# Kernel optimization log

Measured on AMD Instinct MI355X. Metric: run time of the kernel, lower is better.

The kernel has to match this reference:

```python
import jax, jax.numpy as jnp
import numpy as np

DIM = 4096
N_HEADS = 32
N_KV_HEADS = 8
HEAD_DIM = DIM // N_HEADS  # 128
N_REP = N_HEADS // N_KV_HEADS  # 4
MAX_BS = 16
MAX_SEQ = 4096
SEQLEN = 1
START_POS = 4095
ROPE_THETA = 500000.0


def setup_inputs() -> dict:
    key = jax.random.key(0)
    ks = jax.random.split(key, 8)
    w_scale = 0.02  # keep logits in a sane range
    x = jax.random.normal(ks[0], (MAX_BS, SEQLEN, DIM), dtype=jnp.float32)
    wq = jax.random.normal(ks[1], (DIM, N_HEADS * HEAD_DIM), dtype=jnp.float32) * w_scale
    wk = jax.random.normal(ks[2], (DIM, N_KV_HEADS * HEAD_DIM), dtype=jnp.float32) * w_scale
    wv = jax.random.normal(ks[3], (DIM, N_KV_HEADS * HEAD_DIM), dtype=jnp.float32) * w_scale
    wo = jax.random.normal(ks[4], (N_HEADS * HEAD_DIM, DIM), dtype=jnp.float32) * w_scale
    cache_k = jax.random.normal(ks[5], (MAX_BS, MAX_SEQ, N_KV_HEADS, HEAD_DIM), dtype=jnp.float32)
    cache_v = jax.random.normal(ks[6], (MAX_BS, MAX_SEQ, N_KV_HEADS, HEAD_DIM), dtype=jnp.float32)
    # true rotary frequencies for positions [START_POS, START_POS+SEQLEN)
    inv_freq = 1.0 / (ROPE_THETA ** (np.arange(0, HEAD_DIM, 2, dtype=np.float32) / HEAD_DIM))  # [hd/2]
    t = np.arange(START_POS, START_POS + SEQLEN, dtype=np.float32)[:, None]  # [s,1]
    angles = t * inv_freq[None, :]  # [s, hd/2]
    freqs_cos = jnp.asarray(np.cos(angles), dtype=jnp.float32)
    freqs_sin = jnp.asarray(np.sin(angles), dtype=jnp.float32)
    return {"x": x, "wq": wq, "wk": wk, "wv": wv, "wo": wo,
            "cache_k": cache_k, "cache_v": cache_v,
            "freqs_cos": freqs_cos, "freqs_sin": freqs_sin,
            "start_pos": START_POS}


def _rope(t, cos, sin):
    # t: [b, s, h, hd]; cos/sin: [s, hd/2] -> broadcast [1, s, 1, hd/2]
    b, s, h, hd = t.shape
    tp = t.reshape(b, s, h, hd // 2, 2)
    e, o = tp[..., 0], tp[..., 1]
    c = cos[None, :, None, :]
    sn = sin[None, :, None, :]
    re = e * c - o * sn
    im = e * sn + o * c
    return jnp.stack([re, im], axis=-1).reshape(b, s, h, hd)


def reference(x, wq, wk, wv, wo, cache_k, cache_v, freqs_cos, freqs_sin, start_pos):
    bsz, seqlen, _ = x.shape
    xq = (x @ wq).reshape(bsz, seqlen, N_HEADS, HEAD_DIM)
    xk = (x @ wk).reshape(bsz, seqlen, N_KV_HEADS, HEAD_DIM)
    xv = (x @ wv).reshape(bsz, seqlen, N_KV_HEADS, HEAD_DIM)
    xq = _rope(xq, freqs_cos, freqs_sin)
    xk = _rope(xk, freqs_cos, freqs_sin)
    # KV-cache append
    cache_k = jax.lax.dynamic_update_slice(cache_k, xk, (0, start_pos, 0, 0))
    cache_v = jax.lax.dynamic_update_slice(cache_v, xv, (0, start_pos, 0, 0))
    kv_len = start_pos + seqlen  # static Python int
    keys = cache_k[:, :kv_len]    # [b, t, g, hd]
    values = cache_v[:, :kv_len]  # [b, t, g, hd]
    # GQA via broadcasting (math-equivalent to repeat_kv)
    q = xq.reshape(bsz, seqlen, N_KV_HEADS, N_REP, HEAD_DIM)
    scale = 1.0 / jnp.sqrt(jnp.float32(HEAD_DIM))
    scores = jnp.einsum('bsgrh,btgh->bgrst', q, keys) * scale  # [b,g,r,s,t]
    probs = jax.nn.softmax(scores.astype(jnp.float32), axis=-1).astype(xq.dtype)
    out = jnp.einsum('bgrst,btgh->bsgrh', probs, values)  # [b,s,g,r,hd]
    out = out.reshape(bsz, seqlen, N_HEADS * HEAD_DIM)
    return out @ wo
```

## Files before the change

kernel.cpp:

```cpp
#include <hip/hip_runtime.h>
#include <math.h>

#define DIM    4096
#define NH     32
#define NKV    8
#define HD     128
#define BS     16
#define KVLEN  4096
#define LASTPOS 4095
#define QKV_COLS 6144
#define SS_STR 520

#define WS_QKV   0
#define WS_ATTN  98304
#define WS_PART  163840

__global__ __launch_bounds__(256) void zero_ws(
    float* __restrict__ qkv, float* __restrict__ out) {
  int i = blockIdx.x * 256 + threadIdx.x;
  float4 z = make_float4(0.f, 0.f, 0.f, 0.f);
  if (i < 24576) ((float4*)qkv)[i] = z;
  else           ((float4*)out)[i - 24576] = z;
}

__global__ __launch_bounds__(256) void qkv_proj(
    const float* __restrict__ x, const float* __restrict__ wq,
    const float* __restrict__ wk, const float* __restrict__ wv,
    float* __restrict__ qkv) {
  __shared__ float xs[16 * 64];
  const int tid = threadIdx.x;
  const int col = (blockIdx.x * 256 + tid) * 2;
  const int k0 = blockIdx.y * 64;

  for (int i = tid; i < 1024; i += 256) {
    int b = i >> 6, k = i & 63;
    xs[i] = x[b * DIM + k0 + k];
  }
  __syncthreads();

  const float* w;
  int wstride, wcol;
  if (col < 4096)      { w = wq; wstride = 4096; wcol = col; }
  else if (col < 5120) { w = wk; wstride = 1024; wcol = col - 4096; }
  else                 { w = wv; wstride = 1024; wcol = col - 5120; }
  const float* wp = w + (size_t)k0 * wstride + wcol;

  float acc0[16], acc1[16];
#pragma unroll
  for (int b = 0; b < 16; ++b) { acc0[b] = 0.f; acc1[b] = 0.f; }

#pragma unroll 2
  for (int k = 0; k < 64; k += 4) {
    float2 w0 = *(const float2*)(wp + (size_t)(k + 0) * wstride);
    float2 w1 = *(const float2*)(wp + (size_t)(k + 1) * wstride);
    float2 w2 = *(const float2*)(wp + (size_t)(k + 2) * wstride);
    float2 w3 = *(const float2*)(wp + (size_t)(k + 3) * wstride);
#pragma unroll
    for (int b = 0; b < 16; ++b) {
      float4 xb = *(const float4*)(&xs[b * 64 + k]);
      acc0[b] += xb.x * w0.x + xb.y * w1.x + xb.z * w2.x + xb.w * w3.x;
      acc1[b] += xb.x * w0.y + xb.y * w1.y + xb.z * w2.y + xb.w * w3.y;
    }
  }
#pragma unroll
  for (int b = 0; b < 16; ++b) {
    atomicAdd(&qkv[b * QKV_COLS + col],     acc0[b]);
    atomicAdd(&qkv[b * QKV_COLS + col + 1], acc1[b]);
  }
}

__global__ __launch_bounds__(256) void rope_kernel(
    float* __restrict__ qkv, const float* __restrict__ fc,
    const float* __restrict__ fs) {
  int t = blockIdx.x * 256 + threadIdx.x;
  if (t >= 16 * 40 * 64) return;
  int i  = t & 63;
  int hh = (t >> 6) % 40;
  int b  = t / (40 * 64);
  float c = fc[i], s = fs[i];
  int base;
  float scale;
  if (hh < 32) { base = b * QKV_COLS + hh * 128 + 2 * i; scale = 0.08838834764831845f; }
  else         { base = b * QKV_COLS + 4096 + (hh - 32) * 128 + 2 * i; scale = 1.0f; }
  float e = qkv[base], o = qkv[base + 1];
  qkv[base]     = (e * c - o * s) * scale;
  qkv[base + 1] = (e * s + o * c) * scale;
}

__global__ __launch_bounds__(512, 4) void attn_partial(
    const float* __restrict__ cache_k, const float* __restrict__ cache_v,
    const float* __restrict__ qkv, float* __restrict__ part) {
  __shared__ float qs[512];
  __shared__ float ss[4 * SS_STR];
  __shared__ float pacc[8][4][128];
  const int tid = threadIdx.x;
  const int w = tid >> 6, lane = tid & 63;
  const int p = lane >> 4, ql = lane & 15;
  const int chunk = blockIdx.x & 7;
  const int bg = blockIdx.x >> 3;
  const int b = bg >> 3, g = bg & 7;

  qs[tid] = qkv[b * QKV_COLS + g * 512 + tid];
  __syncthreads();

  float4 qA[4], qB[4];
#pragma unroll
  for (int h = 0; h < 4; ++h) {
    qA[h] = *(const float4*)(&qs[h * 128 + ql * 8]);
    qB[h] = *(const float4*)(&qs[h * 128 + ql * 8 + 4]);
  }

  const int t0 = chunk * 512;
  const float* kbase = cache_k + ((size_t)b * 4096 * 8 + g) * 128;
  const float* xk    = qkv + b * QKV_COLS + 4096 + g * 128;

  for (int it = 0; it < 16; ++it) {
    int r = w * 64 + it * 4 + p;
    int t = t0 + r;
    const float* krow = (t == LASTPOS) ? xk : (kbase + (size_t)t * 1024);
    float4 k0 = *(const float4*)(krow + ql * 8);
    float4 k1 = *(const float4*)(krow + ql * 8 + 4);
    float s[4];
#pragma unroll
    for (int h = 0; h < 4; ++h) {
      s[h] = k0.x * qA[h].x + k0.y * qA[h].y + k0.z * qA[h].z + k0.w * qA[h].w
           + k1.x * qB[h].x + k1.y * qB[h].y + k1.z * qB[h].z + k1.w * qB[h].w;
    }
#pragma unroll
    for (int off = 1; off < 16; off <<= 1) {
#pragma unroll
      for (int h = 0; h < 4; ++h) s[h] += __shfl_xor(s[h], off);
    }
    float v = (ql == 0) ? s[0] : (ql == 1) ? s[1] : (ql == 2) ? s[2] : s[3];
    if (ql < 4) ss[ql * SS_STR + r] = v;
  }
  __syncthreads();

  float* prow = part + ((size_t)(bg * 8 + chunk) * 4 + (w & 3)) * 130;
  if (w < 4) {
    float vals[8];
    float m = -1e30f;
#pragma unroll
    for (int i = 0; i < 8; ++i) {
      vals[i] = ss[w * SS_STR + lane + 64 * i];
      m = fmaxf(m, vals[i]);
    }
#pragma unroll
    for (int off = 1; off < 64; off <<= 1) m = fmaxf(m, __shfl_xor(m, off));
    float l = 0.f;
#pragma unroll
    for (int i = 0; i < 8; ++i) {
      float pe = __expf(vals[i] - m);
      ss[w * SS_STR + lane + 64 * i] = pe;
      l += pe;
    }
#pragma unroll
    for (int off = 1; off < 64; off <<= 1) l += __shfl_xor(l, off);
    if (lane == 0) { prow[128] = m; prow[129] = l; }
  }
  __syncthreads();

  const float* vbase = cache_v + ((size_t)b * 4096 * 8 + g) * 128;
  const float* xv    = qkv + b * QKV_COLS + 5120 + g * 128;
  const int h2 = lane >> 5;
  const int dq = lane & 31;
  float4 acc[4];
#pragma unroll
  for (int h = 0; h < 4; ++h) acc[h] = make_float4(0.f, 0.f, 0.f, 0.f);

#pragma unroll 2
  for (int j = 0; j < 32; ++j) {
    int r = w * 64 + 2 * j + h2;
    int t = t0 + r;
    const float* vrow = (t == LASTPOS) ? xv : (vbase + (size_t)t * 1024);
    float4 vv = *(const float4*)(vrow + dq * 4);
    float p0 = ss[0 * SS_STR + r];
    float p1 = ss[1 * SS_STR + r];
    float p2 = ss[2 * SS_STR + r];
    float p3 = ss[3 * SS_STR + r];
    acc[0].x += p0 * vv.x; acc[0].y += p0 * vv.y; acc[0].z += p0 * vv.z; acc[0].w += p0 * vv.w;
    acc[1].x += p1 * vv.x; acc[1].y += p1 * vv.y; acc[1].z += p1 * vv.z; acc[1].w += p1 * vv.w;
    acc[2].x += p2 * vv.x; acc[2].y += p2 * vv.y; acc[2].z += p2 * vv.z; acc[2].w += p2 * vv.w;
    acc[3].x += p3 * vv.x; acc[3].y += p3 * vv.y; acc[3].z += p3 * vv.z; acc[3].w += p3 * vv.w;
  }
#pragma unroll
  for (int h = 0; h < 4; ++h) {
    acc[h].x += __shfl_xor(acc[h].x, 32);
    acc[h].y += __shfl_xor(acc[h].y, 32);
    acc[h].z += __shfl_xor(acc[h].z, 32);
    acc[h].w += __shfl_xor(acc[h].w, 32);
  }
  if (lane < 32) {
#pragma unroll
    for (int h = 0; h < 4; ++h)
      *(float4*)(&pacc[w][h][dq * 4]) = acc[h];
  }
  __syncthreads();

  {
    int h = tid >> 7, d = tid & 127;
    float sum = 0.f;
#pragma unroll
    for (int w2 = 0; w2 < 8; ++w2) sum += pacc[w2][h][d];
    part[((size_t)(bg * 8 + chunk) * 4 + h) * 130 + d] = sum;
  }
}

__global__ __launch_bounds__(256) void attn_combine(
    const float* __restrict__ part, float* __restrict__ attn_out) {
  int t = blockIdx.x * 256 + threadIdx.x;
  int d = t & 127, r = (t >> 7) & 3, bg = t >> 9;
  int b = bg >> 3, g = bg & 7;
  float ms[8];
  float M = -1e30f;
#pragma unroll
  for (int c = 0; c < 8; ++c) {
    ms[c] = part[((size_t)(bg * 8 + c) * 4 + r) * 130 + 128];
    M = fmaxf(M, ms[c]);
  }
  float num = 0.f, den = 0.f;
#pragma unroll
  for (int c = 0; c < 8; ++c) {
    const float* prow = part + ((size_t)(bg * 8 + c) * 4 + r) * 130;
    float wgt = __expf(ms[c] - M);
    num += wgt * prow[d];
    den += wgt * prow[129];
  }
  attn_out[b * DIM + (g * 4 + r) * 128 + d] = num / den;
}

__global__ __launch_bounds__(256) void out_proj(
    const float* __restrict__ attn, const float* __restrict__ wo,
    float* __restrict__ out) {
  __shared__ float xs[16 * 64];
  const int tid = threadIdx.x;
  const int col = blockIdx.x * 256 + tid;
  const int k0 = blockIdx.y * 64;

  for (int i = tid; i < 1024; i += 256) {
    int b = i >> 6, k = i & 63;
    xs[i] = attn[b * DIM + k0 + k];
  }
  __syncthreads();

  const float* wp = wo + (size_t)k0 * 4096 + col;
  float acc[16];
#pragma unroll
  for (int b = 0; b < 16; ++b) acc[b] = 0.f;

#pragma unroll 2
  for (int k = 0; k < 64; k += 4) {
    float w0 = wp[(size_t)(k + 0) * 4096];
    float w1 = wp[(size_t)(k + 1) * 4096];
    float w2 = wp[(size_t)(k + 2) * 4096];
    float w3 = wp[(size_t)(k + 3) * 4096];
#pragma unroll
    for (int b = 0; b < 16; ++b) {
      float4 xb = *(const float4*)(&xs[b * 64 + k]);
      acc[b] += xb.x * w0 + xb.y * w1 + xb.z * w2 + xb.w * w3;
    }
  }
#pragma unroll
  for (int b = 0; b < 16; ++b) atomicAdd(&out[b * DIM + col], acc[b]);
}

extern "C" void kernel_launch(void* const* d_in, const int* in_sizes, int n_in,
                              void* d_out, int out_size, void* d_ws, size_t ws_size,
                              hipStream_t stream) {
  const float* x  = (const float*)d_in[0];
  const float* wq = (const float*)d_in[1];
  const float* wk = (const float*)d_in[2];
  const float* wv = (const float*)d_in[3];
  const float* wo = (const float*)d_in[4];
  const float* ck = (const float*)d_in[5];
  const float* cv = (const float*)d_in[6];
  const float* fc = (const float*)d_in[7];
  const float* fs = (const float*)d_in[8];

  float* ws_f  = (float*)d_ws;
  float* qkv   = ws_f + WS_QKV;
  float* attn  = ws_f + WS_ATTN;
  float* part  = ws_f + WS_PART;
  float* out   = (float*)d_out;

  zero_ws<<<160, 256, 0, stream>>>(qkv, out);
  qkv_proj<<<dim3(12, 64), 256, 0, stream>>>(x, wq, wk, wv, qkv);
  rope_kernel<<<160, 256, 0, stream>>>(qkv, fc, fs);
  attn_partial<<<1024, 512, 0, stream>>>(ck, cv, qkv, part);
  attn_combine<<<256, 256, 0, stream>>>(part, attn);
  out_proj<<<dim3(16, 64), 256, 0, stream>>>(attn, wo, out);
}
```

Measured before the change: 202.8 us.

## Replace atomic split-K with partial buffers and reduce kernels, halve attention chunk

```diff
diff --git a/kernel.cpp b/kernel.cpp
--- a/kernel.cpp
+++ b/kernel.cpp
@@ -9,28 +9,26 @@
 #define KVLEN  4096
 #define LASTPOS 4095
 #define QKV_COLS 6144
-#define SS_STR 520
+#define CHUNK  256
+#define NCH    16
+#define SS_STR 264
+#define NKC    64
 
 #define WS_QKV   0
 #define WS_ATTN  98304
 #define WS_PART  163840
-
-__global__ __launch_bounds__(256) void zero_ws(
-    float* __restrict__ qkv, float* __restrict__ out) {
-  int i = blockIdx.x * 256 + threadIdx.x;
-  float4 z = make_float4(0.f, 0.f, 0.f, 0.f);
-  if (i < 24576) ((float4*)qkv)[i] = z;
-  else           ((float4*)out)[i - 24576] = z;
-}
-
-__global__ __launch_bounds__(256) void qkv_proj(
+#define WS_PQ    1228800
+#define WS_PW    7520256
+
+__global__ __launch_bounds__(256) void qkv_projA(
     const float* __restrict__ x, const float* __restrict__ wq,
     const float* __restrict__ wk, const float* __restrict__ wv,
-    float* __restrict__ qkv) {
+    float* __restrict__ pq) {
   __shared__ float xs[16 * 64];
   const int tid = threadIdx.x;
   const int col = (blockIdx.x * 256 + tid) * 2;
-  const int k0 = blockIdx.y * 64;
+  const int kc = blockIdx.y;
+  const int k0 = kc * 64;
 
   for (int i = tid; i < 1024; i += 256) {
     int b = i >> 6, k = i & 63;
@@ -64,30 +62,34 @@
   }
 #pragma unroll
   for (int b = 0; b < 16; ++b) {
-    atomicAdd(&qkv[b * QKV_COLS + col],     acc0[b]);
-    atomicAdd(&qkv[b * QKV_COLS + col + 1], acc1[b]);
-  }
-}
-
-__global__ __launch_bounds__(256) void rope_kernel(
-    float* __restrict__ qkv, const float* __restrict__ fc,
-    const float* __restrict__ fs) {
+    *(float2*)(&pq[((size_t)kc * 16 + b) * QKV_COLS + col]) = make_float2(acc0[b], acc1[b]);
+  }
+}
+
+__global__ __launch_bounds__(256) void qkv_projB(
+    const float* __restrict__ pq, float* __restrict__ qkv,
+    const float* __restrict__ fc, const float* __restrict__ fs) {
   int t = blockIdx.x * 256 + threadIdx.x;
-  if (t >= 16 * 40 * 64) return;
-  int i  = t & 63;
-  int hh = (t >> 6) % 40;
-  int b  = t / (40 * 64);
-  float c = fc[i], s = fs[i];
-  int base;
-  float scale;
-  if (hh < 32) { base = b * QKV_COLS + hh * 128 + 2 * i; scale = 0.08838834764831845f; }
-  else         { base = b * QKV_COLS + 4096 + (hh - 32) * 128 + 2 * i; scale = 1.0f; }
-  float e = qkv[base], o = qkv[base + 1];
-  qkv[base]     = (e * c - o * s) * scale;
-  qkv[base + 1] = (e * s + o * c) * scale;
-}
-
-__global__ __launch_bounds__(512, 4) void attn_partial(
+  int b = t / 3072, pr = t % 3072;
+  int col = 2 * pr;
+  float e = 0.f, o = 0.f;
+#pragma unroll 8
+  for (int kc = 0; kc < NKC; ++kc) {
+    float2 v = *(const float2*)(&pq[((size_t)kc * 16 + b) * QKV_COLS + col]);
+    e += v.x; o += v.y;
+  }
+  float re = e, im = o;
+  if (col < 5120) {
+    int i = (col & 127) >> 1;
+    float c = fc[i], s = fs[i];
+    float scale = (col < 4096) ? 0.08838834764831845f : 1.0f;
+    re = (e * c - o * s) * scale;
+    im = (e * s + o * c) * scale;
+  }
+  *(float2*)(&qkv[b * QKV_COLS + col]) = make_float2(re, im);
+}
+
+__global__ __launch_bounds__(512, 8) void attn_partial(
     const float* __restrict__ cache_k, const float* __restrict__ cache_v,
     const float* __restrict__ qkv, float* __restrict__ part) {
   __shared__ float qs[512];
@@ -96,8 +98,8 @@
   const int tid = threadIdx.x;
   const int w = tid >> 6, lane = tid & 63;
   const int p = lane >> 4, ql = lane & 15;
-  const int chunk = blockIdx.x & 7;
-  const int bg = blockIdx.x >> 3;
+  const int chunk = blockIdx.x & 15;
+  const int bg = blockIdx.x >> 4;
   const int b = bg >> 3, g = bg & 7;
 
   qs[tid] = qkv[b * QKV_COLS + g * 512 + tid];
@@ -110,12 +112,13 @@
     qB[h] = *(const float4*)(&qs[h * 128 + ql * 8 + 4]);
   }
 
-  const int t0 = chunk * 512;
+  const int t0 = chunk * CHUNK;
   const float* kbase = cache_k + ((size_t)b * 4096 * 8 + g) * 128;
   const float* xk    = qkv + b * QKV_COLS + 4096 + g * 128;
 
-  for (int it = 0; it < 16; ++it) {
-    int r = w * 64 + it * 4 + p;
+#pragma unroll 1
+  for (int it = 0; it < 8; ++it) {
+    int r = w * 32 + it * 4 + p;
     int t = t0 + r;
     const float* krow = (t == LASTPOS) ? xk : (kbase + (size_t)t * 1024);
     float4 k0 = *(const float4*)(krow + ql * 8);
@@ -136,12 +139,12 @@
   }
   __syncthreads();
 
-  float* prow = part + ((size_t)(bg * 8 + chunk) * 4 + (w & 3)) * 130;
+  float* prow = part + ((size_t)(bg * NCH + chunk) * 4 + (w & 3)) * 130;
   if (w < 4) {
-    float vals[8];
+    float vals[4];
     float m = -1e30f;
 #pragma unroll
-    for (int i = 0; i < 8; ++i) {
+    for (int i = 0; i < 4; ++i) {
       vals[i] = ss[w * SS_STR + lane + 64 * i];
       m = fmaxf(m, vals[i]);
     }
@@ -149,7 +152,7 @@
     for (int off = 1; off < 64; off <<= 1) m = fmaxf(m, __shfl_xor(m, off));
     float l = 0.f;
 #pragma unroll
-    for (int i = 0; i < 8; ++i) {
+    for (int i = 0; i < 4; ++i) {
       float pe = __expf(vals[i] - m);
       ss[w * SS_STR + lane + 64 * i] = pe;
       l += pe;
@@ -168,9 +171,9 @@
 #pragma unroll
   for (int h = 0; h < 4; ++h) acc[h] = make_float4(0.f, 0.f, 0.f, 0.f);
 
-#pragma unroll 2
-  for (int j = 0; j < 32; ++j) {
-    int r = w * 64 + 2 * j + h2;
+#pragma unroll 4
+  for (int j = 0; j < 16; ++j) {
+    int r = w * 32 + 2 * j + h2;
     int t = t0 + r;
     const float* vrow = (t == LASTPOS) ? xv : (vbase + (size_t)t * 1024);
     float4 vv = *(const float4*)(vrow + dq * 4);
@@ -202,7 +205,7 @@
     float sum = 0.f;
 #pragma unroll
     for (int w2 = 0; w2 < 8; ++w2) sum += pacc[w2][h][d];
-    part[((size_t)(bg * 8 + chunk) * 4 + h) * 130 + d] = sum;
+    part[((size_t)(bg * NCH + chunk) * 4 + h) * 130 + d] = sum;
   }
 }
 
@@ -211,17 +214,17 @@
   int t = blockIdx.x * 256 + threadIdx.x;
   int d = t & 127, r = (t >> 7) & 3, bg = t >> 9;
   int b = bg >> 3, g = bg & 7;
-  float ms[8];
   float M = -1e30f;
-#pragma unroll
-  for (int c = 0; c < 8; ++c) {
-    ms[c] = part[((size_t)(bg * 8 + c) * 4 + r) * 130 + 128];
+  float ms[NCH];
+#pragma unroll
+  for (int c = 0; c < NCH; ++c) {
+    ms[c] = part[((size_t)(bg * NCH + c) * 4 + r) * 130 + 128];
     M = fmaxf(M, ms[c]);
   }
   float num = 0.f, den = 0.f;
 #pragma unroll
-  for (int c = 0; c < 8; ++c) {
-    const float* prow = part + ((size_t)(bg * 8 + c) * 4 + r) * 130;
+  for (int c = 0; c < NCH; ++c) {
+    const float* prow = part + ((size_t)(bg * NCH + c) * 4 + r) * 130;
     float wgt = __expf(ms[c] - M);
     num += wgt * prow[d];
     den += wgt * prow[129];
@@ -229,13 +232,14 @@
   attn_out[b * DIM + (g * 4 + r) * 128 + d] = num / den;
 }
 
-__global__ __launch_bounds__(256) void out_proj(
+__global__ __launch_bounds__(256) void out_projA(
     const float* __restrict__ attn, const float* __restrict__ wo,
-    float* __restrict__ out) {
+    float* __restrict__ pw) {
   __shared__ float xs[16 * 64];
   const int tid = threadIdx.x;
-  const int col = blockIdx.x * 256 + tid;
-  const int k0 = blockIdx.y * 64;
+  const int col = (blockIdx.x * 256 + tid) * 2;
+  const int kc = blockIdx.y;
+  const int k0 = kc * 64;
 
   for (int i = tid; i < 1024; i += 256) {
     int b = i >> 6, k = i & 63;
@@ -244,24 +248,38 @@
   __syncthreads();
 
   const float* wp = wo + (size_t)k0 * 4096 + col;
-  float acc[16];
-#pragma unroll
-  for (int b = 0; b < 16; ++b) acc[b] = 0.f;
+  float acc0[16], acc1[16];
+#pragma unroll
+  for (int b = 0; b < 16; ++b) { acc0[b] = 0.f; acc1[b] = 0.f; }
 
 #pragma unroll 2
   for (int k = 0; k < 64; k += 4) {
-    float w0 = wp[(size_t)(k + 0) * 4096];
-    float w1 = wp[(size_t)(k + 1) * 4096];
-    float w2 = wp[(size_t)(k + 2) * 4096];
-    float w3 = wp[(size_t)(k + 3) * 4096];
+    float2 w0 = *(const float2*)(wp + (size_t)(k + 0) * 4096);
+    float2 w1 = *(const float2*)(wp + (size_t)(k + 1) * 4096);
+    float2 w2 = *(const float2*)(wp + (size_t)(k + 2) * 4096);
+    float2 w3 = *(const float2*)(wp + (size_t)(k + 3) * 4096);
 #pragma unroll
     for (int b = 0; b < 16; ++b) {
       float4 xb = *(const float4*)(&xs[b * 64 + k]);
-      acc[b] += xb.x * w0 + xb.y * w1 + xb.z * w2 + xb.w * w3;
-    }
-  }
-#pragma unroll
-  for (int b = 0; b < 16; ++b) atomicAdd(&out[b * DIM + col], acc[b]);
+      acc0[b] += xb.x * w0.x + xb.y * w1.x + xb.z * w2.x + xb.w * w3.x;
+      acc1[b] += xb.x * w0.y + xb.y * w1.y + xb.z * w2.y + xb.w * w3.y;
+    }
+  }
+#pragma unroll
+  for (int b = 0; b < 16; ++b) {
+    *(float2*)(&pw[((size_t)kc * 16 + b) * DIM + col]) = make_float2(acc0[b], acc1[b]);
+  }
+}
+
+__global__ __launch_bounds__(256) void out_projB(
+    const float* __restrict__ pw, float* __restrict__ out) {
+  int t = blockIdx.x * 256 + threadIdx.x;
+  int b = t >> 12, col = t & 4095;
+  float sum = 0.f;
+#pragma unroll 8
+  for (int kc = 0; kc < NKC; ++kc)
+    sum += pw[((size_t)kc * 16 + b) * DIM + col];
+  out[b * DIM + col] = sum;
 }
 
 extern "C" void kernel_launch(void* const* d_in, const int* in_sizes, int n_in,
@@ -281,12 +299,14 @@
   float* qkv   = ws_f + WS_QKV;
   float* attn  = ws_f + WS_ATTN;
   float* part  = ws_f + WS_PART;
+  float* pq    = ws_f + WS_PQ;
+  float* pw    = ws_f + WS_PW;
   float* out   = (float*)d_out;
 
-  zero_ws<<<160, 256, 0, stream>>>(qkv, out);
-  qkv_proj<<<dim3(12, 64), 256, 0, stream>>>(x, wq, wk, wv, qkv);
-  rope_kernel<<<160, 256, 0, stream>>>(qkv, fc, fs);
-  attn_partial<<<1024, 512, 0, stream>>>(ck, cv, qkv, part);
+  qkv_projA<<<dim3(12, NKC), 256, 0, stream>>>(x, wq, wk, wv, pq);
+  qkv_projB<<<192, 256, 0, stream>>>(pq, qkv, fc, fs);
+  attn_partial<<<2048, 512, 0, stream>>>(ck, cv, qkv, part);
   attn_combine<<<256, 256, 0, stream>>>(part, attn);
-  out_proj<<<dim3(16, 64), 256, 0, stream>>>(attn, wo, out);
-}
+  out_projA<<<dim3(8, NKC), 256, 0, stream>>>(attn, wo, pw);
+  out_projB<<<256, 256, 0, stream>>>(pw, out);
+}
```

Result: faster. 185.4 us (-8.6%).
